# Optimization experiments

Hardware: AMD Instinct MI355X
Metric: run time of the kernel (lower is better)

The kernel has to match this reference:

```python
import jax, jax.numpy as jnp
import numpy as np

N = 4096; E = 65536; F_IN = 500; H = 64; RATIO = 0.8
K1 = int(np.ceil(RATIO * N))      # 3277
K2 = int(np.ceil(RATIO * K1))     # 2622
K3 = int(np.ceil(RATIO * K2))     # 2098


def _dense_adj(edge_index, n):
    # A[dst, src] = 1 for each edge (PyG source->target flow), then add_remaining_self_loops
    A = jnp.zeros((n, n), jnp.float32).at[edge_index[1], edge_index[0]].set(1.0)
    return A.at[jnp.diag_indices(n)].set(1.0)


def _gcn(A, x, W, b):
    # GCNConv: D^-1/2 (A + I) D^-1/2 @ (x @ W) + b  (edge weights are all 1 here)
    n = A.shape[0]
    A = A.at[jnp.diag_indices(n)].set(1.0)
    d = A.sum(axis=1)
    dis = jnp.where(d > 0, jax.lax.rsqrt(d), 0.0)
    An = dis[:, None] * A * dis[None, :]
    return An @ (x @ W) + b


def _score(A, x, w_rel, b_rel, w_root):
    # SAGPooling default GraphConv scorer: W_rel * sum_j x_j + b_rel + W_root * x_i
    return ((A @ x) @ w_rel + b_rel + x @ w_root)[:, 0]


def _pool(A, x, s, k):
    # topk by score, gate kept features with tanh(score), filter adjacency to kept nodes
    vals, idx = jax.lax.top_k(s, k)
    return x[idx] * jnp.tanh(vals)[:, None], A[idx][:, idx], idx


def _augment(A):
    # augment_adj: spspmm(A, A) = A^2; edge weights are discarded so result is binary
    return (A @ A > 0).astype(A.dtype)


def setup_inputs() -> dict:
    key = jax.random.key(0)
    ks = jax.random.split(key, 16)
    g = lambda k, shp: jax.random.normal(k, shp, jnp.float32) / np.sqrt(shp[0])
    z = lambda shp: jnp.zeros(shp, jnp.float32)
    return {
        "x": jax.random.normal(ks[0], (N, F_IN), jnp.float32),
        "w1": g(ks[1], (F_IN, H)), "b1": z((H,)),
        "w2": g(ks[2], (H, H)), "b2": z((H,)),
        "w3": g(ks[3], (H, H)), "b3": z((H,)),
        "p1_wrel": g(ks[4], (H, 1)), "p1_brel": z((1,)), "p1_wroot": g(ks[5], (H, 1)),
        "p2_wrel": g(ks[6], (H, 1)), "p2_brel": z((1,)), "p2_wroot": g(ks[7], (H, 1)),
        "p3_wrel": g(ks[8], (H, 1)), "p3_brel": z((1,)), "p3_wroot": g(ks[9], (H, 1)),
        "u0_w": g(ks[10], (H, H)), "u0_b": z((H,)),
        "u1_w": g(ks[11], (H, H)), "u1_b": z((H,)),
        "u2_w": g(ks[12], (H, F_IN)), "u2_b": z((F_IN,)),
        "edge_index": jax.random.randint(ks[13], (2, E), 0, N),
    }


def reference(x, w1, b1, w2, b2, w3, b3,
              p1_wrel, p1_brel, p1_wroot,
              p2_wrel, p2_brel, p2_wroot,
              p3_wrel, p3_brel, p3_wroot,
              u0_w, u0_b, u1_w, u1_b, u2_w, u2_b,
              edge_index):
    A0 = _dense_adj(edge_index, N)                 # edge_index + self loops
    # encoder: conv -> SAGPool -> augment (A^2), x3
    x1 = _gcn(A0, x, w1, b1)
    x1p, A1, perm1 = _pool(A0, x1, _score(A0, x1, p1_wrel, p1_brel, p1_wroot), K1)
    A1a = _augment(A1)
    x2 = _gcn(A1a, x1p, w2, b2)
    x2p, A2, perm2 = _pool(A1a, x2, _score(A1a, x2, p2_wrel, p2_brel, p2_wroot), K2)
    A2a = _augment(A2)
    x3 = _gcn(A2a, x2p, w3, b3)
    x3p, A3, perm3 = _pool(A2a, x3, _score(A2a, x3, p3_wrel, p3_brel, p3_wroot), K3)
    # decoder: scatter-unpool (up[perm] = z) then conv on the stored adjacency
    z = x3p
    up = jnp.zeros((K2, H), x.dtype).at[perm3].set(z)
    z = jax.nn.relu(_gcn(A2a, up, u0_w, u0_b))
    up = jnp.zeros((K1, H), x.dtype).at[perm2].set(z)
    z = jax.nn.relu(_gcn(A1a, up, u1_w, u1_b))
    up = jnp.zeros((N, H), x.dtype).at[perm1].set(z)
    z = _gcn(A0, up, u2_w, u2_b)
    return z
```

## Files before the change

kernel.cpp:

```cpp
#include <hip/hip_runtime.h>


constexpr int NN  = 4096;
constexpr int EE  = 65536;
constexpr int FIN = 500;
constexpr int KK1 = 3277, KK2 = 2622, KK3 = 2098;
constexpr int W0  = 128;
constexpr int W1  = (KK1 + 31) / 32;
constexpr int W2  = (KK2 + 31) / 32;
constexpr int CAP = 2048;


__global__ void fill4_kernel(float4* p, long n4) {
  long i = (long)blockIdx.x * blockDim.x + threadIdx.x;
  long stride = (long)gridDim.x * blockDim.x;
  float4 z = make_float4(0.f, 0.f, 0.f, 0.f);
  for (; i < n4; i += stride) p[i] = z;
}

__global__ void scatter_bits_kernel(unsigned* Ab, const int* __restrict__ ei) {
  int e = blockIdx.x * 256 + threadIdx.x;
  if (e < EE) {
    int src = ei[e], dst = ei[EE + e];
    atomicOr(&Ab[(size_t)dst * W0 + (src >> 5)], 1u << (src & 31));
  }
  if (e < NN) atomicOr(&Ab[(size_t)e * W0 + (e >> 5)], 1u << (e & 31));
}

__global__ void popcnt_dis_kernel(const unsigned* __restrict__ bits, int Wd,
                                  float* dis, int M) {
  int lane = threadIdx.x & 63;
  int row = blockIdx.x * 4 + (threadIdx.x >> 6);
  if (row >= M) return;
  const unsigned* rb = bits + (size_t)row * Wd;
  int c = 0;
  for (int w = lane; w < Wd; w += 64) c += __popc(rb[w]);
  for (int off = 32; off; off >>= 1) c += __shfl_down(c, off, 64);
  if (!lane) dis[row] = c > 0 ? rsqrtf((float)c) : 0.f;
}

__global__ void spmm_nbr_kernel(const unsigned* __restrict__ bits, int Wd,
                                const float* __restrict__ B,
                                const float* __restrict__ base,
                                const float* __restrict__ rowscale,
                                const float* __restrict__ bias,
                                const float* __restrict__ wrel,
                                const float* __restrict__ wroot,
                                float* __restrict__ tvec, float* __restrict__ rvec,
                                const int* __restrict__ sperm,
                                const float* __restrict__ sscale,
                                float* __restrict__ C, int M, int relu) {
  __shared__ int nbr[4][CAP];
  __shared__ int cnt[4];
  int lane = threadIdx.x & 63, wv = threadIdx.x >> 6;
  int row = blockIdx.x * 4 + wv;
  if (threadIdx.x < 4) cnt[threadIdx.x] = 0;
  __syncthreads();
  if (row < M) {
    const unsigned* rb = bits + (size_t)row * Wd;
    for (int w = lane; w < Wd; w += 64) {
      unsigned m = rb[w];
      while (m) {
        int b = __ffs(m) - 1;
        m &= m - 1;
        int idx = atomicAdd(&cnt[wv], 1);
        if (idx < CAP) nbr[wv][idx] = (w << 5) + b;
      }
    }
  }
  __syncthreads();
  if (row >= M) return;
  int nc = cnt[wv];
  float acc;
  if (nc <= CAP) {
    const int* lst = nbr[wv];
    float a0 = 0.f, a1 = 0.f, a2 = 0.f, a3 = 0.f;
    int q = 0;
    for (; q + 8 <= nc; q += 8) {
      int j0 = lst[q],     j1 = lst[q + 1], j2 = lst[q + 2], j3 = lst[q + 3];
      int j4 = lst[q + 4], j5 = lst[q + 5], j6 = lst[q + 6], j7 = lst[q + 7];
      float v0 = B[(size_t)j0 * 64 + lane], v1 = B[(size_t)j1 * 64 + lane];
      float v2 = B[(size_t)j2 * 64 + lane], v3 = B[(size_t)j3 * 64 + lane];
      float v4 = B[(size_t)j4 * 64 + lane], v5 = B[(size_t)j5 * 64 + lane];
      float v6 = B[(size_t)j6 * 64 + lane], v7 = B[(size_t)j7 * 64 + lane];
      a0 += v0 + v4; a1 += v1 + v5; a2 += v2 + v6; a3 += v3 + v7;
    }
    for (; q < nc; q++) a0 += B[(size_t)lst[q] * 64 + lane];
    acc = (a0 + a1) + (a2 + a3);
  } else {
    const unsigned* rb = bits + (size_t)row * Wd;
    float a = 0.f;
    for (int w = 0; w < Wd; w++) {
      unsigned m = rb[w];
      while (m) {
        int b = __ffs(m) - 1;
        m &= m - 1;
        a += B[(size_t)((w << 5) + b) * 64 + lane];
      }
    }
    acc = a;
  }
  if (base) acc = base[lane] - acc;
  float v = acc * rowscale[row];
  if (bias) v += bias[lane];
  if (relu) v = fmaxf(v, 0.f);
  if (sperm) {
    int p = sperm[row];
    C[(size_t)p * 64 + lane] = v * sscale[p];
  } else {
    C[(size_t)row * 64 + lane] = v;
  }
  if (wrel) {
    float t1 = v * wrel[lane], t2 = v * wroot[lane];
    for (int off = 32; off; off >>= 1) {
      t1 += __shfl_down(t1, off, 64);
      t2 += __shfl_down(t2, off, 64);
    }
    if (!lane) { tvec[row] = t1; rvec[row] = t2; }
  }
}

__global__ void matvec_bits_kernel(const unsigned* __restrict__ bits, int Wd,
                                   const float* __restrict__ t,
                                   const float* __restrict__ rv,
                                   const float* __restrict__ brel,
                                   const float* __restrict__ total,
                                   float* __restrict__ s,
                                   int* __restrict__ rankz, int M) {
  int lane = threadIdx.x & 63;
  int row = blockIdx.x * 4 + (threadIdx.x >> 6);
  if (row >= M) return;
  const unsigned* rb = bits + (size_t)row * Wd;
  float acc = 0.f;
  for (int w = lane; w < Wd; w += 64) {
    unsigned m = rb[w];
    while (m) {
      int b = __ffs(m) - 1;
      m &= m - 1;
      acc += t[(w << 5) + b];
    }
  }
  for (int off = 32; off; off >>= 1) acc += __shfl_down(acc, off, 64);
  if (!lane) {
    float r0 = total ? total[0] - acc : acc;
    s[row] = r0 + brel[0] + rv[row];
    rankz[row] = 0;
  }
}

__global__ void vec_total_kernel(const float* __restrict__ t, int n, float* tot) {
  __shared__ float red[256];
  float a = 0.f;
  for (int i = threadIdx.x; i < n; i += 256) a += t[i];
  red[threadIdx.x] = a;
  __syncthreads();
  for (int o = 128; o; o >>= 1) {
    if (threadIdx.x < o) red[threadIdx.x] += red[threadIdx.x + o];
    __syncthreads();
  }
  if (!threadIdx.x) tot[0] = red[0];
}

__global__ void topk_count_kernel(const float* __restrict__ s, int n, int* rank) {
  __shared__ float sh[512];
  int j0 = blockIdx.y * 512;
  for (int j = threadIdx.x; j < 512; j += 256) {
    int gj = j0 + j;
    sh[j] = gj < n ? s[gj] : 0.f;
  }
  __syncthreads();
  int i = blockIdx.x * 256 + threadIdx.x;
  if (i >= n) return;
  float si = s[i];
  int jmax = min(512, n - j0);
  int cnt = 0;
  for (int j = 0; j < jmax; j++) {
    float sj = sh[j];
    int gj = j0 + j;
    cnt += (sj > si || (sj == si && gj < i)) ? 1 : 0;
  }
  if (cnt) atomicAdd(&rank[i], cnt);
}

__global__ void topk_place_kernel(const float* __restrict__ s,
                                  const int* __restrict__ rank, int n, int k,
                                  int* perm, float* vals) {
  int i = blockIdx.x * 256 + threadIdx.x;
  if (i >= n) return;
  int rk = rank[i];
  if (rk < k) { perm[rk] = i; vals[rk] = s[i]; }
}

__global__ void scatter_gate_kernel(const float* __restrict__ X,
                                    const int* __restrict__ perm,
                                    const float* __restrict__ vals,
                                    const float* __restrict__ scale,
                                    float* up, int k) {
  int r = blockIdx.x * 4 + (threadIdx.x >> 6);
  int f = threadIdx.x & 63;
  if (r < k) {
    int p = perm[r];
    up[(size_t)p * 64 + f] = X[(size_t)p * 64 + f] * tanhf(vals[r]) * scale[p];
  }
}

__global__ void subgraph_bits_kernel(const unsigned* __restrict__ Ab, int WdIn,
                                     const int* __restrict__ perm, int K, int WdOut,
                                     unsigned* __restrict__ out) {
  __shared__ unsigned rowb[128];
  int r = blockIdx.x;
  const unsigned* src = Ab + (size_t)perm[r] * WdIn;
  for (int w = threadIdx.x; w < WdIn; w += 256) rowb[w] = src[w];
  __syncthreads();
  unsigned* ob = out + (size_t)r * WdOut;
  for (int c0 = 0; c0 < WdOut * 32; c0 += 256) {
    int c = c0 + threadIdx.x;
    bool pred = false;
    if (c < K) {
      int pc = perm[c];
      pred = (rowb[pc >> 5] >> (pc & 31)) & 1u;
    }
    unsigned long long m = __ballot(pred);
    if ((threadIdx.x & 63) == 0) {
      int wb = (c0 >> 5) + ((threadIdx.x >> 6) << 1);
      if (wb < WdOut)     ob[wb]     = (unsigned)m;
      if (wb + 1 < WdOut) ob[wb + 1] = (unsigned)(m >> 32);
    }
  }
}

__global__ void augment_or_kernel(const unsigned* __restrict__ in,
                                  unsigned* __restrict__ out,
                                  unsigned* __restrict__ holes,
                                  float* __restrict__ dis, int Wd, int K) {
  __shared__ unsigned roww[128];
  __shared__ int nbr[CAP];
  __shared__ int cnt;
  __shared__ int pcred[128];
  int i = blockIdx.x;
  if (threadIdx.x == 0) cnt = 0;
  const unsigned* rin = in + (size_t)i * Wd;
  for (int w = threadIdx.x; w < Wd; w += 128) roww[w] = rin[w];
  __syncthreads();
  for (int w = threadIdx.x; w < Wd; w += 128) {
    unsigned m = roww[w];
    while (m) {
      int b = __ffs(m) - 1;
      m &= m - 1;
      int idx = atomicAdd(&cnt, 1);
      if (idx < CAP) nbr[idx] = w * 32 + b;
    }
  }
  __syncthreads();
  int nc = min(cnt, CAP);
  int pc = 0;
  for (int w = threadIdx.x; w < Wd; w += 128) {
    unsigned a0 = 0, a1 = 0, a2 = 0, a3 = 0;
    int q = 0;
    for (; q + 4 <= nc; q += 4) {
      a0 |= in[(size_t)nbr[q] * Wd + w];
      a1 |= in[(size_t)nbr[q + 1] * Wd + w];
      a2 |= in[(size_t)nbr[q + 2] * Wd + w];
      a3 |= in[(size_t)nbr[q + 3] * Wd + w];
    }
    for (; q < nc; q++) a0 |= in[(size_t)nbr[q] * Wd + w];
    unsigned acc = (a0 | a1) | (a2 | a3);
    pc += __popc(acc);
    if (out) out[(size_t)i * Wd + w] = acc;
    if (holes) {
      int valid = K - w * 32;
      unsigned mask = valid >= 32 ? 0xffffffffu : ((1u << valid) - 1u);
      holes[(size_t)i * Wd + w] = ~acc & mask;
    }
  }
  pcred[threadIdx.x] = pc;
  __syncthreads();
  for (int o = 64; o; o >>= 1) {
    if (threadIdx.x < o) pcred[threadIdx.x] += pcred[threadIdx.x + o];
    __syncthreads();
  }
  if (!threadIdx.x) dis[i] = pcred[0] > 0 ? rsqrtf((float)pcred[0]) : 0.f;
}

__global__ __launch_bounds__(256) void gemm500_kernel(
    const float* __restrict__ A, const float* __restrict__ B,
    float* __restrict__ part) {
  __shared__ float As[32][68];
  __shared__ float Bs[32][68];
  int tr = threadIdx.x >> 4, tc = threadIdx.x & 15;
  int row0 = blockIdx.x * 64;
  int k0 = blockIdx.y * 125;
  float c00 = 0.f, c01 = 0.f, c02 = 0.f, c03 = 0.f;
  float c10 = 0.f, c11 = 0.f, c12 = 0.f, c13 = 0.f;
  float c20 = 0.f, c21 = 0.f, c22 = 0.f, c23 = 0.f;
  float c30 = 0.f, c31 = 0.f, c32 = 0.f, c33 = 0.f;
  int ra = tr * 4, cb = tc * 4;
  for (int c0 = 0; c0 < 125; c0 += 32) {
    for (int l = threadIdx.x; l < 64 * 32; l += 256) {
      int r = l >> 5, kk = l & 31;
      int gk = c0 + kk;
      As[kk][r] = (gk < 125) ? A[(size_t)(row0 + r) * FIN + k0 + gk] : 0.f;
    }
    for (int l = threadIdx.x; l < 32 * 64; l += 256) {
      int kk = l >> 6, c = l & 63;
      int gk = c0 + kk;
      Bs[kk][c] = (gk < 125) ? B[(size_t)(k0 + gk) * 64 + c] : 0.f;
    }
    __syncthreads();
#pragma unroll
    for (int kk = 0; kk < 32; kk++) {
      float a0 = As[kk][ra + 0], a1 = As[kk][ra + 1];
      float a2 = As[kk][ra + 2], a3 = As[kk][ra + 3];
      float b0 = Bs[kk][cb + 0], b1 = Bs[kk][cb + 1];
      float b2 = Bs[kk][cb + 2], b3 = Bs[kk][cb + 3];
      c00 += a0 * b0; c01 += a0 * b1; c02 += a0 * b2; c03 += a0 * b3;
      c10 += a1 * b0; c11 += a1 * b1; c12 += a1 * b2; c13 += a1 * b3;
      c20 += a2 * b0; c21 += a2 * b1; c22 += a2 * b2; c23 += a2 * b3;
      c30 += a3 * b0; c31 += a3 * b1; c32 += a3 * b2; c33 += a3 * b3;
    }
    __syncthreads();
  }
  float* P = part + (size_t)blockIdx.y * NN * 64;
  size_t base = (size_t)(row0 + ra) * 64 + cb;
  *(float4*)&P[base]            = make_float4(c00, c01, c02, c03);
  *(float4*)&P[base + 64]       = make_float4(c10, c11, c12, c13);
  *(float4*)&P[base + 128]      = make_float4(c20, c21, c22, c23);
  *(float4*)&P[base + 192]      = make_float4(c30, c31, c32, c33);
}

__global__ void reduce4_scale_kernel(const float4* __restrict__ part,
                                     const float* __restrict__ rowscale,
                                     float4* __restrict__ outp) {
  int e = blockIdx.x * 256 + threadIdx.x;
  if (e >= NN * 16) return;
  float4 v0 = part[e];
  float4 v1 = part[e + NN * 16];
  float4 v2 = part[e + 2 * NN * 16];
  float4 v3 = part[e + 3 * NN * 16];
  float s = rowscale[e >> 4];
  float4 r;
  r.x = (v0.x + v1.x + v2.x + v3.x) * s;
  r.y = (v0.y + v1.y + v2.y + v3.y) * s;
  r.z = (v0.z + v1.z + v2.z + v3.z) * s;
  r.w = (v0.w + v1.w + v2.w + v3.w) * s;
  outp[e] = r;
}

__global__ __launch_bounds__(256) void gemm_k64x4_kernel(
    const float* __restrict__ X, const float* __restrict__ B,
    const int* __restrict__ perm, const float* __restrict__ vals,
    const float* __restrict__ gscale, float* __restrict__ C, int M) {
  __shared__ float Bs[64][65];
  __shared__ float As2[64][20];
  __shared__ int   srcs[16];
  __shared__ float gates[16];
  int t = threadIdx.x;
  int c = t & 63, g = t >> 6;
  int r0 = blockIdx.x * 16;
  if (t < 16) {
    int row = r0 + t;
    int src = 0; float gt = 1.f;
    if (row < M) {
      src = row;
      if (perm) { src = perm[row]; gt = tanhf(vals[row]) * gscale[row]; }
    }
    srcs[t] = src; gates[t] = gt;
  }
  for (int l = t; l < 64 * 64; l += 256) Bs[l >> 6][l & 63] = B[l];
  __syncthreads();
  for (int l = t; l < 16 * 64; l += 256) {
    int rr = l >> 6, k = l & 63;
    int p = (rr & 3) * 4 + (rr >> 2);
    As2[k][p] = (r0 + rr < M) ? X[(size_t)srcs[rr] * 64 + k] * gates[rr] : 0.f;
  }
  __syncthreads();
  float a0 = 0.f, a1 = 0.f, a2 = 0.f, a3 = 0.f;
  int gp = g * 4;
#pragma unroll
  for (int k = 0; k < 64; k++) {
    float x0 = As2[k][gp + 0], x1 = As2[k][gp + 1];
    float x2 = As2[k][gp + 2], x3 = As2[k][gp + 3];
    float bv = Bs[k][c];
    a0 += x0 * bv; a1 += x1 * bv; a2 += x2 * bv; a3 += x3 * bv;
  }
  if (r0 + g      < M) C[(size_t)(r0 + g)      * 64 + c] = a0;
  if (r0 + g + 4  < M) C[(size_t)(r0 + g + 4)  * 64 + c] = a1;
  if (r0 + g + 8  < M) C[(size_t)(r0 + g + 8)  * 64 + c] = a2;
  if (r0 + g + 12 < M) C[(size_t)(r0 + g + 12) * 64 + c] = a3;
}

__global__ void colsum_part_kernel(const float* __restrict__ X, int K,
                                   float* part) {
  __shared__ float red[4][64];
  int lane = threadIdx.x & 63, wv = threadIdx.x >> 6;
  int r0 = blockIdx.x * 64;
  float a = 0.f;
  for (int i = wv; i < 64; i += 4) {
    int r = r0 + i;
    if (r < K) a += X[(size_t)r * 64 + lane];
  }
  red[wv][lane] = a;
  __syncthreads();
  if (!wv)
    part[(size_t)blockIdx.x * 64 + lane] =
        red[0][lane] + red[1][lane] + red[2][lane] + red[3][lane];
}

__global__ void colsum_final_kernel(const float* __restrict__ part, int G,
                                    float* csum) {
  __shared__ float red[4][64];
  int lane = threadIdx.x & 63, wv = threadIdx.x >> 6;
  float a = 0.f;
  for (int g = wv; g < G; g += 4) a += part[(size_t)g * 64 + lane];
  red[wv][lane] = a;
  __syncthreads();
  if (!wv)
    csum[lane] = red[0][lane] + red[1][lane] + red[2][lane] + red[3][lane];
}

__global__ __launch_bounds__(256) void gemm_wide_tile_kernel(
    const float* __restrict__ Y, const float* __restrict__ W,
    const float* __restrict__ bias, float* __restrict__ C) {
  __shared__ float Ys[64][68];
  __shared__ float Ws[64][68];
  int tr = threadIdx.x >> 4, tc = threadIdx.x & 15;
  int row0 = blockIdx.x * 64, c0 = blockIdx.y * 64;
  for (int l = threadIdx.x; l < 64 * 64; l += 256) {
    int r = l >> 6, k = l & 63;
    Ys[k][r] = Y[(size_t)(row0 + r) * 64 + k];
  }
  for (int l = threadIdx.x; l < 64 * 64; l += 256) {
    int k = l >> 6, cc = l & 63;
    int gc = c0 + cc;
    Ws[k][cc] = gc < FIN ? W[(size_t)k * FIN + gc] : 0.f;
  }
  __syncthreads();
  float c00 = 0.f, c01 = 0.f, c02 = 0.f, c03 = 0.f;
  float c10 = 0.f, c11 = 0.f, c12 = 0.f, c13 = 0.f;
  float c20 = 0.f, c21 = 0.f, c22 = 0.f, c23 = 0.f;
  float c30 = 0.f, c31 = 0.f, c32 = 0.f, c33 = 0.f;
  int ra = tr * 4, cb = tc * 4;
#pragma unroll
  for (int kk = 0; kk < 64; kk++) {
    float a0 = Ys[kk][ra + 0], a1 = Ys[kk][ra + 1];
    float a2 = Ys[kk][ra + 2], a3 = Ys[kk][ra + 3];
    float b0 = Ws[kk][cb + 0], b1 = Ws[kk][cb + 1];
    float b2 = Ws[kk][cb + 2], b3 = Ws[kk][cb + 3];
    c00 += a0 * b0; c01 += a0 * b1; c02 += a0 * b2; c03 += a0 * b3;
    c10 += a1 * b0; c11 += a1 * b1; c12 += a1 * b2; c13 += a1 * b3;
    c20 += a2 * b0; c21 += a2 * b1; c22 += a2 * b2; c23 += a2 * b3;
    c30 += a3 * b0; c31 += a3 * b1; c32 += a3 * b2; c33 += a3 * b3;
  }
  int row = row0 + ra;
  int gc0 = c0 + cb;
  if (gc0 + 3 < FIN) {
    float b0 = bias[gc0], b1 = bias[gc0 + 1], b2 = bias[gc0 + 2], b3 = bias[gc0 + 3];
    float* p0 = &C[(size_t)row * FIN + gc0];
    p0[0] = c00 + b0; p0[1] = c01 + b1; p0[2] = c02 + b2; p0[3] = c03 + b3;
    float* p1 = p0 + FIN;
    p1[0] = c10 + b0; p1[1] = c11 + b1; p1[2] = c12 + b2; p1[3] = c13 + b3;
    float* p2 = p1 + FIN;
    p2[0] = c20 + b0; p2[1] = c21 + b1; p2[2] = c22 + b2; p2[3] = c23 + b3;
    float* p3 = p2 + FIN;
    p3[0] = c30 + b0; p3[1] = c31 + b1; p3[2] = c32 + b2; p3[3] = c33 + b3;
  } else {
    if (gc0 + 0 < FIN) { float bv = bias[gc0 + 0];
      C[(size_t)(row+0)*FIN+gc0+0]=c00+bv; C[(size_t)(row+1)*FIN+gc0+0]=c10+bv;
      C[(size_t)(row+2)*FIN+gc0+0]=c20+bv; C[(size_t)(row+3)*FIN+gc0+0]=c30+bv; }
    if (gc0 + 1 < FIN) { float bv = bias[gc0 + 1];
      C[(size_t)(row+0)*FIN+gc0+1]=c01+bv; C[(size_t)(row+1)*FIN+gc0+1]=c11+bv;
      C[(size_t)(row+2)*FIN+gc0+1]=c21+bv; C[(size_t)(row+3)*FIN+gc0+1]=c31+bv; }
    if (gc0 + 2 < FIN) { float bv = bias[gc0 + 2];
      C[(size_t)(row+0)*FIN+gc0+2]=c02+bv; C[(size_t)(row+1)*FIN+gc0+2]=c12+bv;
      C[(size_t)(row+2)*FIN+gc0+2]=c22+bv; C[(size_t)(row+3)*FIN+gc0+2]=c32+bv; }
    if (gc0 + 3 < FIN) { float bv = bias[gc0 + 3];
      C[(size_t)(row+0)*FIN+gc0+3]=c03+bv; C[(size_t)(row+1)*FIN+gc0+3]=c13+bv;
      C[(size_t)(row+2)*FIN+gc0+3]=c23+bv; C[(size_t)(row+3)*FIN+gc0+3]=c33+bv; }
  }
}


extern "C" void kernel_launch(void* const* d_in, const int* in_sizes, int n_in,
                              void* d_out, int out_size, void* d_ws, size_t ws_size,
                              hipStream_t stream) {
  const float* x      = (const float*)d_in[0];
  const float* w1     = (const float*)d_in[1];
  const float* b1     = (const float*)d_in[2];
  const float* w2     = (const float*)d_in[3];
  const float* b2     = (const float*)d_in[4];
  const float* w3     = (const float*)d_in[5];
  const float* b3     = (const float*)d_in[6];
  const float* p1wrel = (const float*)d_in[7];
  const float* p1brel = (const float*)d_in[8];
  const float* p1wroot= (const float*)d_in[9];
  const float* p2wrel = (const float*)d_in[10];
  const float* p2brel = (const float*)d_in[11];
  const float* p2wroot= (const float*)d_in[12];
  const float* p3wrel = (const float*)d_in[13];
  const float* p3brel = (const float*)d_in[14];
  const float* p3wroot= (const float*)d_in[15];
  const float* u0w    = (const float*)d_in[16];
  const float* u0b    = (const float*)d_in[17];
  const float* u1w    = (const float*)d_in[18];
  const float* u1b    = (const float*)d_in[19];
  const float* u2w    = (const float*)d_in[20];
  const float* u2b    = (const float*)d_in[21];
  const int*   ei     = (const int*)d_in[22];
  float* out = (float*)d_out;

  char* wp = (char*)d_ws;
  auto alloc = [&](size_t bytes) -> void* {
    void* p = (void*)wp;
    wp += (bytes + 255) & ~(size_t)255;
    return p;
  };
  unsigned* A0b  = (unsigned*)alloc((size_t)NN  * W0 * 4);
  float* up0  = (float*)alloc((size_t)KK2 * 64 * 4);
  float* up1  = (float*)alloc((size_t)KK1 * 64 * 4);
  float* up2  = (float*)alloc((size_t)NN * 64 * 4);
  char* zero_end = wp;
  unsigned* A1b  = (unsigned*)alloc((size_t)KK1 * W1 * 4);
  unsigned* A1ab = (unsigned*)alloc((size_t)KK1 * W1 * 4);
  unsigned* A2b  = (unsigned*)alloc((size_t)KK2 * W2 * 4);
  unsigned* H2b  = (unsigned*)alloc((size_t)KK2 * W2 * 4);
  float* dis0 = (float*)alloc((size_t)NN * 4);
  float* dis1 = (float*)alloc((size_t)KK1 * 4);
  float* dis2 = (float*)alloc((size_t)KK2 * 4);
  float* xw   = (float*)alloc((size_t)NN * 64 * 4);
  float* x1   = (float*)alloc((size_t)NN * 64 * 4);
  float* x2   = (float*)alloc((size_t)KK1 * 64 * 4);
  float* x3   = (float*)alloc((size_t)KK2 * 64 * 4);
  float* y0   = (float*)alloc((size_t)NN * 64 * 4);
  float* part500 = (float*)alloc((size_t)4 * NN * 64 * 4);
  float* tvec = (float*)alloc((size_t)NN * 4);
  float* rvec = (float*)alloc((size_t)NN * 4);
  float* svec = (float*)alloc((size_t)NN * 4);
  float* vals = (float*)alloc((size_t)NN * 4);
  float* part = (float*)alloc((size_t)64 * 64 * 4);
  float* csum = (float*)alloc((size_t)64 * 4);
  float* tot  = (float*)alloc((size_t)4);
  int* rank  = (int*)alloc((size_t)NN * 4);
  int* perm1 = (int*)alloc((size_t)KK1 * 4);
  int* perm2 = (int*)alloc((size_t)KK2 * 4);
  int* perm3 = (int*)alloc((size_t)KK3 * 4);

  {
    long n4 = (long)(zero_end - (char*)A0b) / 16;
    fill4_kernel<<<2048, 256, 0, stream>>>((float4*)A0b, n4);
  }

  scatter_bits_kernel<<<(EE + 255) / 256, 256, 0, stream>>>(A0b, ei);
  popcnt_dis_kernel<<<NN / 4, 256, 0, stream>>>(A0b, W0, dis0, NN);

  gemm500_kernel<<<dim3(64, 4), 256, 0, stream>>>(x, w1, part500);
  reduce4_scale_kernel<<<NN * 16 / 256, 256, 0, stream>>>(
      (const float4*)part500, dis0, (float4*)xw);
  spmm_nbr_kernel<<<NN / 4, 256, 0, stream>>>(A0b, W0, xw, nullptr, dis0, b1,
      p1wrel, p1wroot, tvec, rvec, nullptr, nullptr, x1, NN, 0);
  matvec_bits_kernel<<<NN / 4, 256, 0, stream>>>(A0b, W0, tvec, rvec, p1brel, nullptr, svec, rank, NN);
  topk_count_kernel<<<dim3((NN + 255) / 256, (NN + 511) / 512), 256, 0, stream>>>(svec, NN, rank);
  topk_place_kernel<<<(NN + 255) / 256, 256, 0, stream>>>(svec, rank, NN, KK1, perm1, vals);
  subgraph_bits_kernel<<<KK1, 256, 0, stream>>>(A0b, W0, perm1, KK1, W1, A1b);
  augment_or_kernel<<<KK1, 128, 0, stream>>>(A1b, A1ab, nullptr, dis1, W1, KK1);

  gemm_k64x4_kernel<<<(KK1 + 15) / 16, 256, 0, stream>>>(x1, w2, perm1, vals, dis1, xw, KK1);
  spmm_nbr_kernel<<<(KK1 + 3) / 4, 256, 0, stream>>>(A1ab, W1, xw, nullptr, dis1, b2,
      p2wrel, p2wroot, tvec, rvec, nullptr, nullptr, x2, KK1, 0);
  matvec_bits_kernel<<<(KK1 + 3) / 4, 256, 0, stream>>>(A1ab, W1, tvec, rvec, p2brel, nullptr, svec, rank, KK1);
  topk_count_kernel<<<dim3((KK1 + 255) / 256, (KK1 + 511) / 512), 256, 0, stream>>>(svec, KK1, rank);
  topk_place_kernel<<<(KK1 + 255) / 256, 256, 0, stream>>>(svec, rank, KK1, KK2, perm2, vals);
  subgraph_bits_kernel<<<KK2, 256, 0, stream>>>(A1ab, W1, perm2, KK2, W2, A2b);
  augment_or_kernel<<<KK2, 128, 0, stream>>>(A2b, nullptr, H2b, dis2, W2, KK2);

  gemm_k64x4_kernel<<<(KK2 + 15) / 16, 256, 0, stream>>>(x2, w3, perm2, vals, dis2, xw, KK2);
  colsum_part_kernel<<<(KK2 + 63) / 64, 256, 0, stream>>>(xw, KK2, part);
  colsum_final_kernel<<<1, 256, 0, stream>>>(part, (KK2 + 63) / 64, csum);
  spmm_nbr_kernel<<<(KK2 + 3) / 4, 256, 0, stream>>>(H2b, W2, xw, csum, dis2, b3,
      p3wrel, p3wroot, tvec, rvec, nullptr, nullptr, x3, KK2, 0);
  vec_total_kernel<<<1, 256, 0, stream>>>(tvec, KK2, tot);
  matvec_bits_kernel<<<(KK2 + 3) / 4, 256, 0, stream>>>(H2b, W2, tvec, rvec, p3brel, tot, svec, rank, KK2);
  topk_count_kernel<<<dim3((KK2 + 255) / 256, (KK2 + 511) / 512), 256, 0, stream>>>(svec, KK2, rank);
  topk_place_kernel<<<(KK2 + 255) / 256, 256, 0, stream>>>(svec, rank, KK2, KK3, perm3, vals);
  scatter_gate_kernel<<<(KK3 + 3) / 4, 256, 0, stream>>>(x3, perm3, vals, dis2, up0, KK3);

  gemm_k64x4_kernel<<<(KK2 + 15) / 16, 256, 0, stream>>>(up0, u0w, nullptr, nullptr, nullptr, xw, KK2);
  colsum_part_kernel<<<(KK2 + 63) / 64, 256, 0, stream>>>(xw, KK2, part);
  colsum_final_kernel<<<1, 256, 0, stream>>>(part, (KK2 + 63) / 64, csum);
  spmm_nbr_kernel<<<(KK2 + 3) / 4, 256, 0, stream>>>(H2b, W2, xw, csum, dis2, u0b,
      nullptr, nullptr, nullptr, nullptr, perm2, dis1, up1, KK2, 1);

  gemm_k64x4_kernel<<<(KK1 + 15) / 16, 256, 0, stream>>>(up1, u1w, nullptr, nullptr, nullptr, xw, KK1);
  spmm_nbr_kernel<<<(KK1 + 3) / 4, 256, 0, stream>>>(A1ab, W1, xw, nullptr, dis1, u1b,
      nullptr, nullptr, nullptr, nullptr, perm1, dis0, up2, KK1, 1);

  spmm_nbr_kernel<<<NN / 4, 256, 0, stream>>>(A0b, W0, up2, nullptr, dis0, nullptr,
      nullptr, nullptr, nullptr, nullptr, nullptr, nullptr, y0, NN, 0);
  gemm_wide_tile_kernel<<<dim3(64, 8), 256, 0, stream>>>(y0, u2w, u2b, out);
}
```

Before: 393.4 us.

## Fold small reduction kernels into consumers and merge top-k count/place

Removes the separate colsum_final and vec_total kernels: each spmm wave now sums the per-block column partials itself, and every matvec block redundantly reduces the full t vector in shared memory. The two-pass top-k (atomic rank count, then placement) becomes one kernel where each block loads all scores into shared memory and counts ranks directly, which also drops the rank zeroing. This cuts about ten launches and their serialization gaps, at the price of redundant per-block reduction work and a full O(n^2) compare per block without the 2D split.

```diff
diff --git a/kernel.cpp b/kernel.cpp
--- a/kernel.cpp
+++ b/kernel.cpp
@@ -41,7 +41,7 @@
 
 __global__ void spmm_nbr_kernel(const unsigned* __restrict__ bits, int Wd,
                                 const float* __restrict__ B,
-                                const float* __restrict__ base,
+                                const float* __restrict__ basePart, int baseG,
                                 const float* __restrict__ rowscale,
                                 const float* __restrict__ bias,
                                 const float* __restrict__ wrel,
@@ -100,7 +100,15 @@
     }
     acc = a;
   }
-  if (base) acc = base[lane] - acc;
+  if (basePart) {
+    float s0 = 0.f, s1 = 0.f, s2 = 0.f, s3 = 0.f;
+    for (int g = 0; g < baseG; g += 4) s0 += basePart[(size_t)g * 64 + lane];
+    for (int g = 1; g < baseG; g += 4) s1 += basePart[(size_t)g * 64 + lane];
+    for (int g = 2; g < baseG; g += 4) s2 += basePart[(size_t)g * 64 + lane];
+    for (int g = 3; g < baseG; g += 4) s3 += basePart[(size_t)g * 64 + lane];
+    float base = ((s0 + s1) + s2) + s3;
+    acc = base - acc;
+  }
   float v = acc * rowscale[row];
   if (bias) v += bias[lane];
   if (relu) v = fmaxf(v, 0.f);
@@ -124,9 +132,22 @@
                                    const float* __restrict__ t,
                                    const float* __restrict__ rv,
                                    const float* __restrict__ brel,
-                                   const float* __restrict__ total,
-                                   float* __restrict__ s,
-                                   int* __restrict__ rankz, int M) {
+                                   int useTotal,
+                                   float* __restrict__ s, int M) {
+  __shared__ float red[256];
+  float tot = 0.f;
+  if (useTotal) {
+    float a = 0.f;
+    for (int i = threadIdx.x; i < M; i += 256) a += t[i];
+    red[threadIdx.x] = a;
+    __syncthreads();
+    for (int o = 128; o; o >>= 1) {
+      if (threadIdx.x < o) red[threadIdx.x] += red[threadIdx.x + o];
+      __syncthreads();
+    }
+    tot = red[0];
+    __syncthreads();
+  }
   int lane = threadIdx.x & 63;
   int row = blockIdx.x * 4 + (threadIdx.x >> 6);
   if (row >= M) return;
@@ -142,53 +163,33 @@
   }
   for (int off = 32; off; off >>= 1) acc += __shfl_down(acc, off, 64);
   if (!lane) {
-    float r0 = total ? total[0] - acc : acc;
+    float r0 = useTotal ? tot - acc : acc;
     s[row] = r0 + brel[0] + rv[row];
-    rankz[row] = 0;
-  }
-}
-
-__global__ void vec_total_kernel(const float* __restrict__ t, int n, float* tot) {
-  __shared__ float red[256];
-  float a = 0.f;
-  for (int i = threadIdx.x; i < n; i += 256) a += t[i];
-  red[threadIdx.x] = a;
-  __syncthreads();
-  for (int o = 128; o; o >>= 1) {
-    if (threadIdx.x < o) red[threadIdx.x] += red[threadIdx.x + o];
-    __syncthreads();
-  }
-  if (!threadIdx.x) tot[0] = red[0];
-}
-
-__global__ void topk_count_kernel(const float* __restrict__ s, int n, int* rank) {
-  __shared__ float sh[512];
-  int j0 = blockIdx.y * 512;
-  for (int j = threadIdx.x; j < 512; j += 256) {
-    int gj = j0 + j;
-    sh[j] = gj < n ? s[gj] : 0.f;
-  }
+  }
+}
+
+__global__ void topk_kernel(const float* __restrict__ s, int n, int k,
+                            int* __restrict__ perm, float* __restrict__ vals) {
+  __shared__ float sh[4096];
+  for (int j = threadIdx.x; j < n; j += 256) sh[j] = s[j];
   __syncthreads();
   int i = blockIdx.x * 256 + threadIdx.x;
   if (i >= n) return;
-  float si = s[i];
-  int jmax = min(512, n - j0);
+  float si = sh[i];
   int cnt = 0;
-  for (int j = 0; j < jmax; j++) {
-    float sj = sh[j];
-    int gj = j0 + j;
-    cnt += (sj > si || (sj == si && gj < i)) ? 1 : 0;
-  }
-  if (cnt) atomicAdd(&rank[i], cnt);
-}
-
-__global__ void topk_place_kernel(const float* __restrict__ s,
-                                  const int* __restrict__ rank, int n, int k,
-                                  int* perm, float* vals) {
-  int i = blockIdx.x * 256 + threadIdx.x;
-  if (i >= n) return;
-  int rk = rank[i];
-  if (rk < k) { perm[rk] = i; vals[rk] = s[i]; }
+  int j = 0;
+  for (; j + 4 <= n; j += 4) {
+    float a = sh[j], b = sh[j + 1], c = sh[j + 2], d = sh[j + 3];
+    cnt += (a > si || (a == si && j     < i)) ? 1 : 0;
+    cnt += (b > si || (b == si && j + 1 < i)) ? 1 : 0;
+    cnt += (c > si || (c == si && j + 2 < i)) ? 1 : 0;
+    cnt += (d > si || (d == si && j + 3 < i)) ? 1 : 0;
+  }
+  for (; j < n; j++) {
+    float a = sh[j];
+    cnt += (a > si || (a == si && j < i)) ? 1 : 0;
+  }
+  if (cnt < k) { perm[cnt] = i; vals[cnt] = si; }
 }
 
 __global__ void scatter_gate_kernel(const float* __restrict__ X,
@@ -404,18 +405,6 @@
   if (!wv)
     part[(size_t)blockIdx.x * 64 + lane] =
         red[0][lane] + red[1][lane] + red[2][lane] + red[3][lane];
-}
-
-__global__ void colsum_final_kernel(const float* __restrict__ part, int G,
-                                    float* csum) {
-  __shared__ float red[4][64];
-  int lane = threadIdx.x & 63, wv = threadIdx.x >> 6;
-  float a = 0.f;
-  for (int g = wv; g < G; g += 4) a += part[(size_t)g * 64 + lane];
-  red[wv][lane] = a;
-  __syncthreads();
-  if (!wv)
-    csum[lane] = red[0][lane] + red[1][lane] + red[2][lane] + red[3][lane];
 }
 
 __global__ __launch_bounds__(256) void gemm_wide_tile_kernel(
@@ -537,13 +526,12 @@
   float* svec = (float*)alloc((size_t)NN * 4);
   float* vals = (float*)alloc((size_t)NN * 4);
   float* part = (float*)alloc((size_t)64 * 64 * 4);
-  float* csum = (float*)alloc((size_t)64 * 4);
-  float* tot  = (float*)alloc((size_t)4);
-  int* rank  = (int*)alloc((size_t)NN * 4);
   int* perm1 = (int*)alloc((size_t)KK1 * 4);
   int* perm2 = (int*)alloc((size_t)KK2 * 4);
   int* perm3 = (int*)alloc((size_t)KK3 * 4);
 
+  const int G2 = (KK2 + 63) / 64;
+
   {
     long n4 = (long)(zero_end - (char*)A0b) / 16;
     fill4_kernel<<<2048, 256, 0, stream>>>((float4*)A0b, n4);
@@ -555,45 +543,39 @@
   gemm500_kernel<<<dim3(64, 4), 256, 0, stream>>>(x, w1, part500);
   reduce4_scale_kernel<<<NN * 16 / 256, 256, 0, stream>>>(
       (const float4*)part500, dis0, (float4*)xw);
-  spmm_nbr_kernel<<<NN / 4, 256, 0, stream>>>(A0b, W0, xw, nullptr, dis0, b1,
+  spmm_nbr_kernel<<<NN / 4, 256, 0, stream>>>(A0b, W0, xw, nullptr, 0, dis0, b1,
       p1wrel, p1wroot, tvec, rvec, nullptr, nullptr, x1, NN, 0);
-  matvec_bits_kernel<<<NN / 4, 256, 0, stream>>>(A0b, W0, tvec, rvec, p1brel, nullptr, svec, rank, NN);
-  topk_count_kernel<<<dim3((NN + 255) / 256, (NN + 511) / 512), 256, 0, stream>>>(svec, NN, rank);
-  topk_place_kernel<<<(NN + 255) / 256, 256, 0, stream>>>(svec, rank, NN, KK1, perm1, vals);
+  matvec_bits_kernel<<<NN / 4, 256, 0, stream>>>(A0b, W0, tvec, rvec, p1brel, 0, svec, NN);
+  topk_kernel<<<(NN + 255) / 256, 256, 0, stream>>>(svec, NN, KK1, perm1, vals);
   subgraph_bits_kernel<<<KK1, 256, 0, stream>>>(A0b, W0, perm1, KK1, W1, A1b);
   augment_or_kernel<<<KK1, 128, 0, stream>>>(A1b, A1ab, nullptr, dis1, W1, KK1);
 
   gemm_k64x4_kernel<<<(KK1 + 15) / 16, 256, 0, stream>>>(x1, w2, perm1, vals, dis1, xw, KK1);
-  spmm_nbr_kernel<<<(KK1 + 3) / 4, 256, 0, stream>>>(A1ab, W1, xw, nullptr, dis1, b2,
+  spmm_nbr_kernel<<<(KK1 + 3) / 4, 256, 0, stream>>>(A1ab, W1, xw, nullptr, 0, dis1, b2,
       p2wrel, p2wroot, tvec, rvec, nullptr, nullptr, x2, KK1, 0);
-  matvec_bits_kernel<<<(KK1 + 3) / 4, 256, 0, stream>>>(A1ab, W1, tvec, rvec, p2brel, nullptr, svec, rank, KK1);
-  topk_count_kernel<<<dim3((KK1 + 255) / 256, (KK1 + 511) / 512), 256, 0, stream>>>(svec, KK1, rank);
-  topk_place_kernel<<<(KK1 + 255) / 256, 256, 0, stream>>>(svec, rank, KK1, KK2, perm2, vals);
+  matvec_bits_kernel<<<(KK1 + 3) / 4, 256, 0, stream>>>(A1ab, W1, tvec, rvec, p2brel, 0, svec, KK1);
+  topk_kernel<<<(KK1 + 255) / 256, 256, 0, stream>>>(svec, KK1, KK2, perm2, vals);
   subgraph_bits_kernel<<<KK2, 256, 0, stream>>>(A1ab, W1, perm2, KK2, W2, A2b);
   augment_or_kernel<<<KK2, 128, 0, stream>>>(A2b, nullptr, H2b, dis2, W2, KK2);
 
   gemm_k64x4_kernel<<<(KK2 + 15) / 16, 256, 0, stream>>>(x2, w3, perm2, vals, dis2, xw, KK2);
-  colsum_part_kernel<<<(KK2 + 63) / 64, 256, 0, stream>>>(xw, KK2, part);
-  colsum_final_kernel<<<1, 256, 0, stream>>>(part, (KK2 + 63) / 64, csum);
-  spmm_nbr_kernel<<<(KK2 + 3) / 4, 256, 0, stream>>>(H2b, W2, xw, csum, dis2, b3,
+  colsum_part_kernel<<<G2, 256, 0, stream>>>(xw, KK2, part);
+  spmm_nbr_kernel<<<(KK2 + 3) / 4, 256, 0, stream>>>(H2b, W2, xw, part, G2, dis2, b3,
       p3wrel, p3wroot, tvec, rvec, nullptr, nullptr, x3, KK2, 0);
-  vec_total_kernel<<<1, 256, 0, stream>>>(tvec, KK2, tot);
-  matvec_bits_kernel<<<(KK2 + 3) / 4, 256, 0, stream>>>(H2b, W2, tvec, rvec, p3brel, tot, svec, rank, KK2);
-  topk_count_kernel<<<dim3((KK2 + 255) / 256, (KK2 + 511) / 512), 256, 0, stream>>>(svec, KK2, rank);
-  topk_place_kernel<<<(KK2 + 255) / 256, 256, 0, stream>>>(svec, rank, KK2, KK3, perm3, vals);
+  matvec_bits_kernel<<<(KK2 + 3) / 4, 256, 0, stream>>>(H2b, W2, tvec, rvec, p3brel, 1, svec, KK2);
+  topk_kernel<<<(KK2 + 255) / 256, 256, 0, stream>>>(svec, KK2, KK3, perm3, vals);
   scatter_gate_kernel<<<(KK3 + 3) / 4, 256, 0, stream>>>(x3, perm3, vals, dis2, up0, KK3);
 
   gemm_k64x4_kernel<<<(KK2 + 15) / 16, 256, 0, stream>>>(up0, u0w, nullptr, nullptr, nullptr, xw, KK2);
-  colsum_part_kernel<<<(KK2 + 63) / 64, 256, 0, stream>>>(xw, KK2, part);
-  colsum_final_kernel<<<1, 256, 0, stream>>>(part, (KK2 + 63) / 64, csum);
-  spmm_nbr_kernel<<<(KK2 + 3) / 4, 256, 0, stream>>>(H2b, W2, xw, csum, dis2, u0b,
+  colsum_part_kernel<<<G2, 256, 0, stream>>>(xw, KK2, part);
+  spmm_nbr_kernel<<<(KK2 + 3) / 4, 256, 0, stream>>>(H2b, W2, xw, part, G2, dis2, u0b,
       nullptr, nullptr, nullptr, nullptr, perm2, dis1, up1, KK2, 1);
 
   gemm_k64x4_kernel<<<(KK1 + 15) / 16, 256, 0, stream>>>(up1, u1w, nullptr, nullptr, nullptr, xw, KK1);
-  spmm_nbr_kernel<<<(KK1 + 3) / 4, 256, 0, stream>>>(A1ab, W1, xw, nullptr, dis1, u1b,
+  spmm_nbr_kernel<<<(KK1 + 3) / 4, 256, 0, stream>>>(A1ab, W1, xw, nullptr, 0, dis1, u1b,
       nullptr, nullptr, nullptr, nullptr, perm1, dis0, up2, KK1, 1);
 
-  spmm_nbr_kernel<<<NN / 4, 256, 0, stream>>>(A0b, W0, up2, nullptr, dis0, nullptr,
+  spmm_nbr_kernel<<<NN / 4, 256, 0, stream>>>(A0b, W0, up2, nullptr, 0, dis0, nullptr,
       nullptr, nullptr, nullptr, nullptr, nullptr, nullptr, y0, NN, 0);
   gemm_wide_tile_kernel<<<dim3(64, 8), 256, 0, stream>>>(y0, u2w, u2b, out);
 }
```

New measurement: 629.8 us. +60.1%, slower.
